# Performance work log

Hardware: AMD Instinct MI355X
Metric: run time of the kernel (lower is better)

The kernel has to match this reference:

```python
import jax, jax.numpy as jnp
import numpy as np
import math

V, D, H, L, T, B = 50257, 1024, 16, 8, 1024, 4
HD = D // H
EPS = 1e-5


def setup_inputs() -> dict:
    key = jax.random.key(0)
    ks = jax.random.split(key, 8)
    s = 0.02
    inp = {
        'context': jax.random.randint(ks[0], (B, T), 0, V, dtype=jnp.int32),
        'targets': jax.random.randint(ks[1], (B, T), 0, V, dtype=jnp.int32),
        'wte': jax.random.normal(ks[2], (V, D), jnp.float32) * s,  # tied with lm_head
        'wpe': jax.random.normal(ks[3], (T, D), jnp.float32) * s,
        'ln1_g': jnp.ones((L, D), jnp.float32), 'ln1_b': jnp.zeros((L, D), jnp.float32),
        'w_attn': jax.random.normal(ks[4], (L, 3 * D, D), jnp.float32) * s,
        'w_proj': jax.random.normal(ks[5], (L, D, D), jnp.float32) * s,
        'ln2_g': jnp.ones((L, D), jnp.float32), 'ln2_b': jnp.zeros((L, D), jnp.float32),
        'w_fc': jax.random.normal(ks[6], (L, 4 * D, D), jnp.float32) * s,
        'w_out': jax.random.normal(ks[7], (L, D, 4 * D), jnp.float32) * s,
        'lnf_g': jnp.ones((D,), jnp.float32), 'lnf_b': jnp.zeros((D,), jnp.float32),
    }
    return inp


def layer_norm(x, g, b):
    mu = jnp.mean(x, axis=-1, keepdims=True)
    var = jnp.var(x, axis=-1, keepdims=True)
    return (x - mu) * jax.lax.rsqrt(var + EPS) * g + b


def attention(x, w_attn, w_proj):
    # x: [B,T,D]; w_attn: [3D,D] (torch Linear convention: y = x @ W^T)
    qkv = x @ w_attn.T  # [B,T,3D]
    q, k, v = jnp.split(qkv, 3, axis=-1)
    q = q.reshape(B, T, H, HD).transpose(0, 2, 1, 3)  # [B,H,T,hd]
    k = k.reshape(B, T, H, HD).transpose(0, 2, 1, 3)
    v = v.reshape(B, T, H, HD).transpose(0, 2, 1, 3)
    att = jnp.einsum('bhtd,bhsd->bhts', q, k) * (1.0 / math.sqrt(HD))
    causal = jnp.tril(jnp.ones((T, T), dtype=bool))
    att = jnp.where(causal, att, -jnp.inf)
    att = jax.nn.softmax(att, axis=-1)
    y = jnp.einsum('bhts,bhsd->bhtd', att, v)
    y = y.transpose(0, 2, 1, 3).reshape(B, T, D)
    return y @ w_proj.T


def mlp(x, w_fc, w_out):
    h = jax.nn.gelu(x @ w_fc.T, approximate=False)  # exact GELU = torch nn.GELU()
    return h @ w_out.T


def reference(context, targets, wte, wpe, ln1_g, ln1_b, w_attn, w_proj,
              ln2_g, ln2_b, w_fc, w_out, lnf_g, lnf_b):
    x = wte[context] + wpe[jnp.arange(T)]  # [B,T,D]
    for i in range(L):
        x = x + attention(layer_norm(x, ln1_g[i], ln1_b[i]), w_attn[i], w_proj[i])
        x = x + mlp(layer_norm(x, ln2_g[i], ln2_b[i]), w_fc[i], w_out[i])
    x = layer_norm(x, lnf_g, lnf_b)
    logits = x @ wte.T  # tied lm_head, [B,T,V]
    # cross entropy with ignore_index=-1
    logp = jax.nn.log_softmax(logits, axis=-1)
    tgt = targets.reshape(-1)
    valid = tgt != -1
    safe_tgt = jnp.where(valid, tgt, 0)
    nll = -jnp.take_along_axis(logp.reshape(-1, V), safe_tgt[:, None], axis=-1)[:, 0]
    loss = jnp.sum(jnp.where(valid, nll, 0.0)) / jnp.maximum(jnp.sum(valid), 1)
    return logits, loss
```

## Files before the change

### kernel.cpp

```cpp
#include <hip/hip_runtime.h>
#include <cstdint>

#define V_SIZE 50257
#define V_PAD  50432
#define NCB    197
#define D_DIM  1024
#define H_NUM  16
#define L_NUM  8
#define T_LEN  1024
#define B_NUM  4
#define HD_DIM 64
#define M_ROWS 4096
#define LN_EPS 1e-5f

typedef __attribute__((ext_vector_type(8))) __bf16 bf16x8;
typedef __attribute__((ext_vector_type(4))) float f32x4;
typedef __attribute__((ext_vector_type(8))) unsigned short u16x8;

__device__ __forceinline__ unsigned short f2bf(float f) {
  unsigned u = __builtin_bit_cast(unsigned, f);
  u += 0x7fffu + ((u >> 16) & 1u);
  return (unsigned short)(u >> 16);
}

__device__ __forceinline__ void gload_lds16(const void* g, void* l) {
  typedef const __attribute__((address_space(1))) unsigned int* gp_t;
  typedef __attribute__((address_space(3))) unsigned int* lp_t;
  __builtin_amdgcn_global_load_lds((gp_t)g, (lp_t)l, 16, 0, 0);
}

__device__ __forceinline__ f32x4 mfma16(bf16x8 a, bf16x8 b, f32x4 c) {
  return __builtin_amdgcn_mfma_f32_16x16x32_bf16(a, b, c, 0, 0, 0);
}

#define BARSB() { __builtin_amdgcn_s_barrier(); __builtin_amdgcn_sched_barrier(0); }
#define SCHB()  __builtin_amdgcn_sched_barrier(0)

__global__ __launch_bounds__(256) void embed_kernel(const int* __restrict__ ctx,
                                                    const float* __restrict__ wte,
                                                    const float* __restrict__ wpe,
                                                    float* __restrict__ x) {
  int i = blockIdx.x * blockDim.x + threadIdx.x;
  if (i >= M_ROWS * D_DIM) return;
  int bt = i / D_DIM, d = i - bt * D_DIM;
  int t = bt & (T_LEN - 1);
  x[i] = wte[(size_t)ctx[bt] * D_DIM + d] + wpe[(size_t)t * D_DIM + d];
}

__global__ __launch_bounds__(256) void conv_layer_kernel(const float* __restrict__ wa,
                                                         const float* __restrict__ wp,
                                                         const float* __restrict__ wf,
                                                         const float* __restrict__ wo,
                                                         unsigned short* __restrict__ oa,
                                                         unsigned short* __restrict__ op,
                                                         unsigned short* __restrict__ of,
                                                         unsigned short* __restrict__ oo) {
  long i = (long)(blockIdx.x * 256 + threadIdx.x) * 8;
  const float* src; unsigned short* dst; long off;
  if (i < 3145728L)      { src = wa; dst = oa; off = i; }
  else if (i < 4194304L) { src = wp; dst = op; off = i - 3145728L; }
  else if (i < 8388608L) { src = wf; dst = of; off = i - 4194304L; }
  else                   { src = wo; dst = oo; off = i - 8388608L; }
  float4 v0 = *(const float4*)(src + off);
  float4 v1 = *(const float4*)(src + off + 4);
  u16x8 o;
  o[0] = f2bf(v0.x); o[1] = f2bf(v0.y); o[2] = f2bf(v0.z); o[3] = f2bf(v0.w);
  o[4] = f2bf(v1.x); o[5] = f2bf(v1.y); o[6] = f2bf(v1.z); o[7] = f2bf(v1.w);
  *(u16x8*)(dst + off) = o;
}

__global__ __launch_bounds__(256) void conv_kernel(const float* __restrict__ in,
                                                   unsigned short* __restrict__ out, long n) {
  long i = (long)(blockIdx.x * 256 + threadIdx.x) * 8;
  if (i >= n) return;
  float4 v0 = *(const float4*)(in + i);
  float4 v1 = *(const float4*)(in + i + 4);
  u16x8 o;
  o[0] = f2bf(v0.x); o[1] = f2bf(v0.y); o[2] = f2bf(v0.z); o[3] = f2bf(v0.w);
  o[4] = f2bf(v1.x); o[5] = f2bf(v1.y); o[6] = f2bf(v1.z); o[7] = f2bf(v1.w);
  *(u16x8*)(out + i) = o;
}

__global__ __launch_bounds__(256) void layernorm_kernel(const float* __restrict__ x,
                                                        const float* __restrict__ g,
                                                        const float* __restrict__ b,
                                                        unsigned short* __restrict__ o) {
  int r = blockIdx.x;
  int tid = threadIdx.x;
  const float* row = x + (size_t)r * D_DIM;
  float4 v = *(const float4*)(row + tid * 4);
  float s  = v.x + v.y + v.z + v.w;
  float s2 = v.x * v.x + v.y * v.y + v.z * v.z + v.w * v.w;
  #pragma unroll
  for (int off = 32; off; off >>= 1) {
    s  += __shfl_xor(s, off);
    s2 += __shfl_xor(s2, off);
  }
  __shared__ float a1[4], a2[4];
  int w = tid >> 6, lane = tid & 63;
  if (lane == 0) { a1[w] = s; a2[w] = s2; }
  __syncthreads();
  s  = a1[0] + a1[1] + a1[2] + a1[3];
  s2 = a2[0] + a2[1] + a2[2] + a2[3];
  float mu  = s * (1.0f / D_DIM);
  float var = s2 * (1.0f / D_DIM) - mu * mu;
  float rs  = rsqrtf(var + LN_EPS);
  int d = tid * 4;
  float4 gv = *(const float4*)(g + d);
  float4 bv = *(const float4*)(b + d);
  ushort4 ov;
  ov.x = f2bf((v.x - mu) * rs * gv.x + bv.x);
  ov.y = f2bf((v.y - mu) * rs * gv.y + bv.y);
  ov.z = f2bf((v.z - mu) * rs * gv.z + bv.z);
  ov.w = f2bf((v.w - mu) * rs * gv.w + bv.w);
  *(ushort4*)(o + (size_t)r * D_DIM + d) = ov;
}

template<int EPI>
__global__ __launch_bounds__(256) void mfma_gemm(const unsigned short* __restrict__ A,
                                                 const unsigned short* __restrict__ W,
                                                 const float* R, void* Cout,
                                                 int K, int ldc, int nreal) {
  __shared__ unsigned short As[128 * 32];
  __shared__ unsigned short Bs[128 * 32];
  const int tid  = threadIdx.x;
  const int wave = tid >> 6, lane = tid & 63;
  const int wr = wave >> 1, wc = wave & 1;
  const long row0 = (long)blockIdx.y * 128;
  const long col0 = (long)blockIdx.x * 128;
  f32x4 acc[4][4] = {};
  const int frow = lane & 15;
  const int fk   = (lane >> 4) * 8;
  const int b0 = wave * 2048 + lane * 16;
  for (int k0 = 0; k0 < K; k0 += 32) {
    #pragma unroll
    for (int c = 0; c < 2; ++c) {
      int b = b0 + c * 1024;
      int r = b >> 6, ke = (b & 63) >> 1;
      gload_lds16(A + (row0 + r) * (long)K + k0 + ke, (char*)As + b);
      gload_lds16(W + (col0 + r) * (long)K + k0 + ke, (char*)Bs + b);
    }
    __syncthreads();
    bf16x8 af[4], bfr[4];
    #pragma unroll
    for (int i = 0; i < 4; ++i)
      af[i] = *(const bf16x8*)(As + (wr * 64 + i * 16 + frow) * 32 + fk);
    #pragma unroll
    for (int j = 0; j < 4; ++j)
      bfr[j] = *(const bf16x8*)(Bs + (wc * 64 + j * 16 + frow) * 32 + fk);
    #pragma unroll
    for (int i = 0; i < 4; ++i)
      #pragma unroll
      for (int j = 0; j < 4; ++j)
        acc[i][j] = mfma16(af[i], bfr[j], acc[i][j]);
    __syncthreads();
  }
  const int crow = (lane >> 4) * 4;
  const int ccol = lane & 15;
  #pragma unroll
  for (int i = 0; i < 4; ++i) {
    #pragma unroll
    for (int r = 0; r < 4; ++r) {
      long row = row0 + wr * 64 + i * 16 + crow + r;
      #pragma unroll
      for (int j = 0; j < 4; ++j) {
        long col = col0 + wc * 64 + j * 16 + ccol;
        float v = acc[i][j][r];
        if (EPI == 1) {
          ((float*)Cout)[row * (long)ldc + col] = v + R[row * (long)ldc + col];
        } else {
          ((float*)Cout)[row * (long)ldc + col] = v;
        }
      }
    }
  }
}

__device__ __forceinline__ void stage_chunk8(const unsigned short* __restrict__ base,
                                             long rbase, int K, long gk,
                                             char* cb, int tid) {
  #pragma unroll
  for (int j = 0; j < 2; ++j) {
    int db = j * 8192 + tid * 16;
    int lb = db ^ (((db >> 7) & 3) << 4);
    long r = lb >> 6;
    int e = (lb & 63) >> 1;
    gload_lds16(base + (rbase + r) * (long)K + gk + e, cb + db);
  }
}

__device__ __forceinline__ bf16x8 rdfrag(const char* cb, int rr, int lhi) {
  int p = (rr << 6) + (lhi << 4);
  p ^= ((rr >> 1) & 3) << 4;
  return *(const bf16x8*)(cb + p);
}

template<int EPI>
__global__ __launch_bounds__(512, 1) void gemm8p(const unsigned short* __restrict__ A,
                                                 const unsigned short* __restrict__ W,
                                                 void* Cout, int K, int ldc, int nreal,
                                                 int nbx, int xcd,
                                                 float* __restrict__ psum) {
  __shared__ char lds[131072];
  const int tid  = threadIdx.x;
  const int lane = tid & 63;
  const int wave = tid >> 6;
  const int wr = wave >> 2, wc = wave & 3;
  const int lhi = lane >> 4, llo = lane & 15;
  int bid = blockIdx.x;
  if (xcd) { int per = (int)gridDim.x >> 3; bid = (bid & 7) * per + (bid >> 3); }
  const int brow = bid % nbx;
  const int bcol = bid / nbx;
  const long row0 = (long)brow * 256;
  const long col0 = (long)bcol * 256;
  char* Ab0 = (char*)lds;
  char* Bb0 = (char*)lds + 65536;
  const int nt = K >> 6;

  stage_chunk8(W, col0, K, 0,  Bb0,         tid);
  stage_chunk8(A, row0, K, 0,  Ab0,         tid);
  stage_chunk8(W, col0, K, 32, Bb0 + 16384, tid);
  stage_chunk8(A, row0, K, 32, Ab0 + 16384, tid);
  stage_chunk8(W, col0, K, 64, Bb0 + 32768, tid);
  stage_chunk8(A, row0, K, 64, Ab0 + 32768, tid);
  stage_chunk8(W, col0, K, 96, Bb0 + 49152, tid);
  asm volatile("s_waitcnt vmcnt(10)" ::: "memory");
  BARSB();

  const int arow  = wr * 128 + llo;
  const int brow_ = wc * 64 + llo;

  bf16x8 aa0[4], aa1[4], bb0[4], bb1[4];
  #pragma unroll
  for (int m = 0; m < 4; ++m) aa0[m] = rdfrag(Ab0, arow + m * 16, lhi);
  #pragma unroll
  for (int n = 0; n < 4; ++n) bb0[n] = rdfrag(Bb0, brow_ + n * 16, lhi);

  f32x4 acc[8][4] = {};
  for (int t = 0; t < nt; ++t) {
    char* Ac = Ab0 + (t & 1) * 32768;
    char* Bc = Bb0 + (t & 1) * 32768;
    char* An = Ab0 + ((t + 1) & 1) * 32768;
    char* Bn = Bb0 + ((t + 1) & 1) * 32768;
    #pragma unroll
    for (int m = 0; m < 4; ++m) aa1[m] = rdfrag(Ac, arow + 64 + m * 16, lhi);
    asm volatile("s_waitcnt lgkmcnt(4)" ::: "memory");
    SCHB();
    if (t + 1 < nt) stage_chunk8(A, row0, K, (long)(t + 1) * 64 + 32, An + 16384, tid);
    __builtin_amdgcn_s_setprio(1);
    #pragma unroll
    for (int m = 0; m < 4; ++m)
      #pragma unroll
      for (int n = 0; n < 4; ++n)
        acc[m][n] = mfma16(aa0[m], bb0[n], acc[m][n]);
    __builtin_amdgcn_s_setprio(0);
    SCHB();
    if (t < nt - 1) { asm volatile("s_waitcnt vmcnt(8)" ::: "memory"); }
    else            { asm volatile("s_waitcnt vmcnt(0)" ::: "memory"); }
    BARSB();
    #pragma unroll
    for (int m = 0; m < 4; ++m) aa0[m] = rdfrag(Ac + 16384, arow + m * 16, lhi);
    #pragma unroll
    for (int n = 0; n < 4; ++n) bb1[n] = rdfrag(Bc + 16384, brow_ + n * 16, lhi);
    asm volatile("s_waitcnt lgkmcnt(8)" ::: "memory");
    SCHB();
    if (t + 2 < nt) stage_chunk8(W, col0, K, (long)(t + 2) * 64, Bc, tid);
    __builtin_amdgcn_s_setprio(1);
    #pragma unroll
    for (int m = 0; m < 4; ++m)
      #pragma unroll
      for (int n = 0; n < 4; ++n)
        acc[m + 4][n] = mfma16(aa1[m], bb0[n], acc[m + 4][n]);
    __builtin_amdgcn_s_setprio(0);
    SCHB();
    BARSB();
    #pragma unroll
    for (int m = 0; m < 4; ++m) aa1[m] = rdfrag(Ac + 16384, arow + 64 + m * 16, lhi);
    asm volatile("s_waitcnt lgkmcnt(4)" ::: "memory");
    SCHB();
    if (t + 2 < nt) stage_chunk8(A, row0, K, (long)(t + 2) * 64, Ac, tid);
    __builtin_amdgcn_s_setprio(1);
    #pragma unroll
    for (int m = 0; m < 4; ++m)
      #pragma unroll
      for (int n = 0; n < 4; ++n)
        acc[m][n] = mfma16(aa0[m], bb1[n], acc[m][n]);
    __builtin_amdgcn_s_setprio(0);
    SCHB();
    if (t <= nt - 3)      { asm volatile("s_waitcnt vmcnt(8)" ::: "memory"); }
    else if (t == nt - 2) { asm volatile("s_waitcnt vmcnt(4)" ::: "memory"); }
    else                  { asm volatile("s_waitcnt vmcnt(0)" ::: "memory"); }
    BARSB();
    if (t + 1 < nt) {
      #pragma unroll
      for (int m = 0; m < 4; ++m) aa0[m] = rdfrag(An, arow + m * 16, lhi);
      #pragma unroll
      for (int n = 0; n < 4; ++n) bb0[n] = rdfrag(Bn, brow_ + n * 16, lhi);
      asm volatile("s_waitcnt lgkmcnt(8)" ::: "memory");
    } else {
      asm volatile("s_waitcnt lgkmcnt(0)" ::: "memory");
    }
    SCHB();
    if (t + 2 < nt) stage_chunk8(W, col0, K, (long)(t + 2) * 64 + 32, Bc + 16384, tid);
    __builtin_amdgcn_s_setprio(1);
    #pragma unroll
    for (int m = 0; m < 4; ++m)
      #pragma unroll
      for (int n = 0; n < 4; ++n)
        acc[m + 4][n] = mfma16(aa1[m], bb1[n], acc[m + 4][n]);
    __builtin_amdgcn_s_setprio(0);
    SCHB();
    BARSB();
  }

  #pragma unroll
  for (int mi = 0; mi < 8; ++mi) {
    #pragma unroll
    for (int rg = 0; rg < 4; ++rg) {
      long row = row0 + wr * 128 + mi * 16 + lhi * 4 + rg;
      #pragma unroll
      for (int n = 0; n < 4; ++n) {
        long col = col0 + wc * 64 + n * 16 + llo;
        float v = acc[mi][n][rg];
        if (EPI == 0) {
          if (col < nreal) ((float*)Cout)[row * (long)ldc + col] = v;
        } else if (EPI == 2) {
          float gl = 0.5f * v * (1.0f + erff(v * 0.70710678118654752440f));
          ((unsigned short*)Cout)[row * (long)ldc + col] = f2bf(gl);
        } else {
          ((unsigned short*)Cout)[row * (long)ldc + col] = f2bf(v);
        }
      }
    }
  }

  if (EPI == 0) {
    float* red = (float*)lds;
    #pragma unroll
    for (int mi = 0; mi < 8; ++mi) {
      #pragma unroll
      for (int rg = 0; rg < 4; ++rg) {
        float e = 0.f;
        #pragma unroll
        for (int n = 0; n < 4; ++n) {
          long col = col0 + wc * 64 + n * 16 + llo;
          if (col < nreal) e += __expf(acc[mi][n][rg]);
        }
        #pragma unroll
        for (int off = 1; off < 16; off <<= 1) e += __shfl_xor(e, off);
        if (llo == 0) {
          int rl = wr * 128 + mi * 16 + lhi * 4 + rg;
          red[rl * 4 + wc] = e;
        }
      }
    }
    __syncthreads();
    if (tid < 256) {
      float s = red[tid * 4 + 0] + red[tid * 4 + 1] + red[tid * 4 + 2] + red[tid * 4 + 3];
      psum[(long)bcol * M_ROWS + row0 + tid] = s;
    }
  }
}

__global__ __launch_bounds__(512) void flash_attn_kernel(const unsigned short* __restrict__ qkv,
                                                         unsigned short* __restrict__ y) {
  __shared__ unsigned short Kls[64 * 64];
  __shared__ unsigned short Vtls[64 * 64];
  __shared__ unsigned short Pls[8][16 * 64];
  const int tid = threadIdx.x, wave = tid >> 6, lane = tid & 63;
  const int qt = blockIdx.x;
  const int h = blockIdx.y & (H_NUM - 1), b = blockIdx.y >> 4;
  const int q0 = qt * 128;
  const int lhi = lane >> 4, llo = lane & 15;

  const int qrow = q0 + wave * 16 + llo;
  const unsigned short* qptr =
      qkv + ((size_t)(b * T_LEN + qrow)) * 3072 + h * HD_DIM + lhi * 8;
  const bf16x8 qa0 = *(const bf16x8*)qptr;
  const bf16x8 qa1 = *(const bf16x8*)(qptr + 32);

  f32x4 o[4] = {};
  float m[4] = {-1e30f, -1e30f, -1e30f, -1e30f};
  float l[4] = {0.f, 0.f, 0.f, 0.f};

  const unsigned short* kg = qkv + (size_t)b * T_LEN * 3072 + D_DIM + h * HD_DIM;
  const unsigned short* vg = kg + D_DIM;

  const int vs0 = ((tid & 255) >> 3) * 2, vd0 = (tid & 7) * 8;
  const int t2 = tid - 256;
  const int krow = (t2 & 255) >> 2, kcol = (t2 & 3) * 16;

  const int ntiles = 2 * qt + 2;
  for (int st = 0; st < ntiles; ++st) {
    const int s0 = st * 64;
    if (tid < 256) {
      const unsigned short* src = vg + (size_t)(s0 + vs0) * 3072 + vd0;
      u16x8 a = *(const u16x8*)src;
      u16x8 c = *(const u16x8*)(src + 3072);
      #pragma unroll
      for (int j = 0; j < 8; ++j) {
        int d = vd0 + j;
        unsigned val = (unsigned)a[j] | ((unsigned)c[j] << 16);
        *(unsigned*)((char*)Vtls + ((d * 128 + vs0 * 2) ^ ((d & 7) << 4))) = val;
      }
    } else {
      const unsigned short* src = kg + (size_t)(s0 + krow) * 3072 + kcol;
      u16x8 a = *(const u16x8*)src;
      u16x8 c = *(const u16x8*)(src + 8);
      int base = krow * 128 + kcol * 2;
      int sw = (krow & 7) << 4;
      *(u16x8*)((char*)Kls + ((base) ^ sw))      = a;
      *(u16x8*)((char*)Kls + ((base + 16) ^ sw)) = c;
    }
    __syncthreads();

    f32x4 s_acc[4] = {};
    #pragma unroll
    for (int kt = 0; kt < 4; ++kt) {
      int kr = kt * 16 + llo;
      int sw = (kr & 7) << 4;
      bf16x8 kb0 = *(const bf16x8*)((char*)Kls + ((kr * 128 + lhi * 16) ^ sw));
      bf16x8 kb1 = *(const bf16x8*)((char*)Kls + ((kr * 128 + 64 + lhi * 16) ^ sw));
      s_acc[kt] = mfma16(qa0, kb0, s_acc[kt]);
      s_acc[kt] = mfma16(qa1, kb1, s_acc[kt]);
    }

    float p[4][4];
    float tmax[4] = {-1e30f, -1e30f, -1e30f, -1e30f};
    const int qg = q0 + wave * 16 + lhi * 4;
    #pragma unroll
    for (int kt = 0; kt < 4; ++kt) {
      int ks = s0 + kt * 16 + llo;
      #pragma unroll
      for (int r = 0; r < 4; ++r) {
        float sv = (ks <= qg + r) ? s_acc[kt][r] * 0.125f : -1e30f;
        p[kt][r] = sv;
        tmax[r] = fmaxf(tmax[r], sv);
      }
    }
    #pragma unroll
    for (int r = 0; r < 4; ++r) {
      #pragma unroll
      for (int off = 1; off < 16; off <<= 1)
        tmax[r] = fmaxf(tmax[r], __shfl_xor(tmax[r], off));
      float mn = fmaxf(m[r], tmax[r]);
      float corr = __expf(m[r] - mn);
      m[r] = mn;
      float ps = 0.f;
      #pragma unroll
      for (int kt = 0; kt < 4; ++kt) {
        p[kt][r] = __expf(p[kt][r] - mn);
        ps += p[kt][r];
      }
      #pragma unroll
      for (int off = 1; off < 16; off <<= 1)
        ps += __shfl_xor(ps, off);
      l[r] = l[r] * corr + ps;
      #pragma unroll
      for (int dt = 0; dt < 4; ++dt) o[dt][r] *= corr;
    }

    unsigned short* pw = Pls[wave];
    #pragma unroll
    for (int r = 0; r < 4; ++r) {
      int q = lhi * 4 + r;
      int sw = (q & 7) << 4;
      #pragma unroll
      for (int kt = 0; kt < 4; ++kt) {
        int k = kt * 16 + llo;
        *(unsigned short*)((char*)pw + ((q * 128 + k * 2) ^ sw)) = f2bf(p[kt][r]);
      }
    }
    asm volatile("s_waitcnt lgkmcnt(0)" ::: "memory");

    int psw = (llo & 7) << 4;
    bf16x8 pa0 = *(const bf16x8*)((char*)pw + ((llo * 128 + lhi * 16) ^ psw));
    bf16x8 pa1 = *(const bf16x8*)((char*)pw + ((llo * 128 + 64 + lhi * 16) ^ psw));
    #pragma unroll
    for (int dt = 0; dt < 4; ++dt) {
      int vr = dt * 16 + llo;
      int sw = (vr & 7) << 4;
      bf16x8 vb0 = *(const bf16x8*)((char*)Vtls + ((vr * 128 + lhi * 16) ^ sw));
      bf16x8 vb1 = *(const bf16x8*)((char*)Vtls + ((vr * 128 + 64 + lhi * 16) ^ sw));
      o[dt] = mfma16(pa0, vb0, o[dt]);
      o[dt] = mfma16(pa1, vb1, o[dt]);
    }
    __syncthreads();
  }

  #pragma unroll
  for (int r = 0; r < 4; ++r) {
    long row = q0 + wave * 16 + lhi * 4 + r;
    float inv = 1.0f / l[r];
    #pragma unroll
    for (int dt = 0; dt < 4; ++dt) {
      long col = h * HD_DIM + dt * 16 + llo;
      y[(row + (size_t)b * T_LEN) * D_DIM + col] = f2bf(o[dt][r] * inv);
    }
  }
}

__global__ __launch_bounds__(256) void loss_combine_kernel(const float* __restrict__ psum,
                                                           const float* __restrict__ logits,
                                                           const int* __restrict__ tgt,
                                                           float* __restrict__ nll,
                                                           float* __restrict__ vld) {
  int r = blockIdx.x * 256 + threadIdx.x;
  float s = 0.f;
  for (int cb = 0; cb < NCB; ++cb) s += psum[(long)cb * M_ROWS + r];
  int tg = tgt[r];
  if (tg != -1) { nll[r] = logf(s) - logits[(size_t)r * V_SIZE + tg]; vld[r] = 1.0f; }
  else          { nll[r] = 0.f;                                       vld[r] = 0.f; }
}

__global__ __launch_bounds__(256) void loss_reduce_kernel(const float* __restrict__ nll,
                                                          const float* __restrict__ vld,
                                                          float* __restrict__ out) {
  int tid = threadIdx.x;
  float s = 0.f, c = 0.f;
  for (int i = tid; i < M_ROWS; i += 256) { s += nll[i]; c += vld[i]; }
  #pragma unroll
  for (int off = 32; off; off >>= 1) { s += __shfl_xor(s, off); c += __shfl_xor(c, off); }
  __shared__ float s1[4], s2[4];
  int w = tid >> 6, lane = tid & 63;
  if (lane == 0) { s1[w] = s; s2[w] = c; }
  __syncthreads();
  if (tid == 0) {
    s = s1[0] + s1[1] + s1[2] + s1[3];
    c = s2[0] + s2[1] + s2[2] + s2[3];
    out[0] = s / fmaxf(c, 1.0f);
  }
}

extern "C" void kernel_launch(void* const* d_in, const int* in_sizes, int n_in,
                              void* d_out, int out_size, void* d_ws, size_t ws_size,
                              hipStream_t stream) {
  const int*   ctx    = (const int*)d_in[0];
  const int*   tgt    = (const int*)d_in[1];
  const float* wte    = (const float*)d_in[2];
  const float* wpe    = (const float*)d_in[3];
  const float* ln1_g  = (const float*)d_in[4];
  const float* ln1_b  = (const float*)d_in[5];
  const float* w_attn = (const float*)d_in[6];
  const float* w_proj = (const float*)d_in[7];
  const float* ln2_g  = (const float*)d_in[8];
  const float* ln2_b  = (const float*)d_in[9];
  const float* w_fc   = (const float*)d_in[10];
  const float* w_out  = (const float*)d_in[11];
  const float* lnf_g  = (const float*)d_in[12];
  const float* lnf_b  = (const float*)d_in[13];

  float* outp   = (float*)d_out;
  float* logits = outp;
  float* loss   = outp + (size_t)M_ROWS * V_SIZE;

  char* ws = (char*)d_ws;
  float*          x      = (float*)(ws + 0);
  unsigned short* xn     = (unsigned short*)(ws + 16777216);
  unsigned short* qkv    = (unsigned short*)(ws + 25165824);
  unsigned short* y      = (unsigned short*)(ws + 50331648);
  unsigned short* h      = (unsigned short*)(ws + 58720256);
  unsigned short* wa_bf  = (unsigned short*)(ws + 92274688);
  unsigned short* wp_bf  = (unsigned short*)(ws + 98566144);
  unsigned short* wf_bf  = (unsigned short*)(ws + 100663296);
  unsigned short* wo_bf  = (unsigned short*)(ws + 109051904);
  unsigned short* wte_bf = (unsigned short*)(ws + 25165824);
  float*          nll    = (float*)(ws + 128450560);
  float*          vld    = (float*)(ws + 128466944);
  float*          psum   = (float*)(ws + 128483328);

  embed_kernel<<<(M_ROWS * D_DIM + 255) / 256, 256, 0, stream>>>(ctx, wte, wpe, x);

  for (int l = 0; l < L_NUM; ++l) {
    conv_layer_kernel<<<6144, 256, 0, stream>>>(
        w_attn + (size_t)l * 3 * D_DIM * D_DIM, w_proj + (size_t)l * D_DIM * D_DIM,
        w_fc + (size_t)l * 4 * D_DIM * D_DIM, w_out + (size_t)l * D_DIM * 4 * D_DIM,
        wa_bf, wp_bf, wf_bf, wo_bf);
    layernorm_kernel<<<M_ROWS, 256, 0, stream>>>(x, ln1_g + l * D_DIM, ln1_b + l * D_DIM, xn);
    gemm8p<3><<<12 * 16, 512, 0, stream>>>(
        xn, wa_bf, qkv, D_DIM, 3 * D_DIM, 3 * D_DIM, 16, 1, nullptr);
    flash_attn_kernel<<<dim3(T_LEN / 128, B_NUM * H_NUM), 512, 0, stream>>>(qkv, y);
    mfma_gemm<1><<<dim3(D_DIM / 128, M_ROWS / 128), 256, 0, stream>>>(
        y, wp_bf, x, x, D_DIM, D_DIM, D_DIM);
    layernorm_kernel<<<M_ROWS, 256, 0, stream>>>(x, ln2_g + l * D_DIM, ln2_b + l * D_DIM, xn);
    gemm8p<2><<<16 * 16, 512, 0, stream>>>(
        xn, wf_bf, h, D_DIM, 4 * D_DIM, 4 * D_DIM, 16, 1, nullptr);
    mfma_gemm<1><<<dim3(D_DIM / 128, M_ROWS / 128), 256, 0, stream>>>(
        h, wo_bf, x, x, 4 * D_DIM, D_DIM, D_DIM);
  }

  layernorm_kernel<<<M_ROWS, 256, 0, stream>>>(x, lnf_g, lnf_b, xn);
  conv_kernel<<<25129, 256, 0, stream>>>(wte, wte_bf, (long)V_SIZE * D_DIM);
  hipMemsetAsync(wte_bf + (size_t)V_SIZE * D_DIM, 0,
                 (size_t)(V_PAD - V_SIZE) * D_DIM * sizeof(unsigned short), stream);
  gemm8p<0><<<NCB * 16, 512, 0, stream>>>(
      xn, wte_bf, logits, D_DIM, V_SIZE, V_SIZE, 16, 1, psum);
  loss_combine_kernel<<<M_ROWS / 256, 256, 0, stream>>>(psum, logits, tgt, nll, vld);
  loss_reduce_kernel<<<1, 256, 0, stream>>>(nll, vld, loss);
}
```

Before: 3.168 ms.

## Prefetch next K/V tile into registers and use nontemporal loads/stores

The attention kernel now loads the next K/V tile from global memory into registers right after the barrier, so that load overlaps the current tile's QK^T and softmax compute instead of stalling at the top of each iteration. The fp32-to-bf16 conversion kernels switch to nontemporal loads, and the fp32 logits store in the GEMM epilogue becomes a nontemporal store. The goal is to hide global latency in attention and keep streaming data from polluting the cache. The cost is extra register pressure in the attention kernel, which may lower occupancy.

```diff
diff --git a/kernel.cpp b/kernel.cpp
--- a/kernel.cpp
+++ b/kernel.cpp
@@ -15,6 +15,7 @@
 
 typedef __attribute__((ext_vector_type(8))) __bf16 bf16x8;
 typedef __attribute__((ext_vector_type(4))) float f32x4;
+typedef __attribute__((ext_vector_type(4))) float fv4;
 typedef __attribute__((ext_vector_type(8))) unsigned short u16x8;
 
 __device__ __forceinline__ unsigned short f2bf(float f) {
@@ -61,11 +62,11 @@
   else if (i < 4194304L) { src = wp; dst = op; off = i - 3145728L; }
   else if (i < 8388608L) { src = wf; dst = of; off = i - 4194304L; }
   else                   { src = wo; dst = oo; off = i - 8388608L; }
-  float4 v0 = *(const float4*)(src + off);
-  float4 v1 = *(const float4*)(src + off + 4);
+  fv4 v0 = __builtin_nontemporal_load((const fv4*)(src + off));
+  fv4 v1 = __builtin_nontemporal_load((const fv4*)(src + off + 4));
   u16x8 o;
-  o[0] = f2bf(v0.x); o[1] = f2bf(v0.y); o[2] = f2bf(v0.z); o[3] = f2bf(v0.w);
-  o[4] = f2bf(v1.x); o[5] = f2bf(v1.y); o[6] = f2bf(v1.z); o[7] = f2bf(v1.w);
+  o[0] = f2bf(v0[0]); o[1] = f2bf(v0[1]); o[2] = f2bf(v0[2]); o[3] = f2bf(v0[3]);
+  o[4] = f2bf(v1[0]); o[5] = f2bf(v1[1]); o[6] = f2bf(v1[2]); o[7] = f2bf(v1[3]);
   *(u16x8*)(dst + off) = o;
 }
 
@@ -73,11 +74,11 @@
                                                    unsigned short* __restrict__ out, long n) {
   long i = (long)(blockIdx.x * 256 + threadIdx.x) * 8;
   if (i >= n) return;
-  float4 v0 = *(const float4*)(in + i);
-  float4 v1 = *(const float4*)(in + i + 4);
+  fv4 v0 = __builtin_nontemporal_load((const fv4*)(in + i));
+  fv4 v1 = __builtin_nontemporal_load((const fv4*)(in + i + 4));
   u16x8 o;
-  o[0] = f2bf(v0.x); o[1] = f2bf(v0.y); o[2] = f2bf(v0.z); o[3] = f2bf(v0.w);
-  o[4] = f2bf(v1.x); o[5] = f2bf(v1.y); o[6] = f2bf(v1.z); o[7] = f2bf(v1.w);
+  o[0] = f2bf(v0[0]); o[1] = f2bf(v0[1]); o[2] = f2bf(v0[2]); o[3] = f2bf(v0[3]);
+  o[4] = f2bf(v1[0]); o[5] = f2bf(v1[1]); o[6] = f2bf(v1[2]); o[7] = f2bf(v1[3]);
   *(u16x8*)(out + i) = o;
 }
 
@@ -323,7 +324,8 @@
         long col = col0 + wc * 64 + n * 16 + llo;
         float v = acc[mi][n][rg];
         if (EPI == 0) {
-          if (col < nreal) ((float*)Cout)[row * (long)ldc + col] = v;
+          if (col < nreal)
+            __builtin_nontemporal_store(v, &((float*)Cout)[row * (long)ldc + col]);
         } else if (EPI == 2) {
           float gl = 0.5f * v * (1.0f + erff(v * 0.70710678118654752440f));
           ((unsigned short*)Cout)[row * (long)ldc + col] = f2bf(gl);
@@ -391,29 +393,47 @@
   const int krow = (t2 & 255) >> 2, kcol = (t2 & 3) * 16;
 
   const int ntiles = 2 * qt + 2;
+
+  u16x8 ra, rc;
+  if (tid < 256) {
+    const unsigned short* src = vg + (size_t)vs0 * 3072 + vd0;
+    ra = *(const u16x8*)src;
+    rc = *(const u16x8*)(src + 3072);
+  } else {
+    const unsigned short* src = kg + (size_t)krow * 3072 + kcol;
+    ra = *(const u16x8*)src;
+    rc = *(const u16x8*)(src + 8);
+  }
+
   for (int st = 0; st < ntiles; ++st) {
-    const int s0 = st * 64;
     if (tid < 256) {
-      const unsigned short* src = vg + (size_t)(s0 + vs0) * 3072 + vd0;
-      u16x8 a = *(const u16x8*)src;
-      u16x8 c = *(const u16x8*)(src + 3072);
       #pragma unroll
       for (int j = 0; j < 8; ++j) {
         int d = vd0 + j;
-        unsigned val = (unsigned)a[j] | ((unsigned)c[j] << 16);
+        unsigned val = (unsigned)ra[j] | ((unsigned)rc[j] << 16);
         *(unsigned*)((char*)Vtls + ((d * 128 + vs0 * 2) ^ ((d & 7) << 4))) = val;
       }
     } else {
-      const unsigned short* src = kg + (size_t)(s0 + krow) * 3072 + kcol;
-      u16x8 a = *(const u16x8*)src;
-      u16x8 c = *(const u16x8*)(src + 8);
       int base = krow * 128 + kcol * 2;
       int sw = (krow & 7) << 4;
-      *(u16x8*)((char*)Kls + ((base) ^ sw))      = a;
-      *(u16x8*)((char*)Kls + ((base + 16) ^ sw)) = c;
+      *(u16x8*)((char*)Kls + ((base) ^ sw))      = ra;
+      *(u16x8*)((char*)Kls + ((base + 16) ^ sw)) = rc;
     }
     __syncthreads();
-
+    if (st + 1 < ntiles) {
+      const int s1 = (st + 1) * 64;
+      if (tid < 256) {
+        const unsigned short* src = vg + (size_t)(s1 + vs0) * 3072 + vd0;
+        ra = *(const u16x8*)src;
+        rc = *(const u16x8*)(src + 3072);
+      } else {
+        const unsigned short* src = kg + (size_t)(s1 + krow) * 3072 + kcol;
+        ra = *(const u16x8*)src;
+        rc = *(const u16x8*)(src + 8);
+      }
+    }
+
+    const int s0 = st * 64;
     f32x4 s_acc[4] = {};
     #pragma unroll
     for (int kt = 0; kt < 4; ++kt) {
```

Result: no change. 3.155 ms (-0.4%).
